# Optimization experiments

Measured on AMD Instinct MI355X. Metric: run time of the kernel, lower is better.

## Reference

```python
import jax, jax.numpy as jnp
import numpy as np

H_G, W_G = 9, 25
N_NODES = H_G * W_G  # 225


def _grid_edge_index():
    # 8-connected grid graph INCLUDING self loops (di=dj=0), matching build_grid_edge_index.
    # PyG GATConv's remove_self_loops+add_self_loops leaves this edge set unchanged.
    edges = []
    for i in range(H_G):
        for j in range(W_G):
            nid = i * W_G + j
            for di in (-1, 0, 1):
                for dj in (-1, 0, 1):
                    ni, nj = i + di, j + dj
                    if 0 <= ni < H_G and 0 <= nj < W_G:
                        edges.append((nid, ni * W_G + nj))
    return jnp.asarray(np.array(edges, dtype=np.int32).T)  # [2, 1825]


def _gat(x, edge_index, W, a_src, a_dst, bias, concat):
    # x: [B, N, F_in]; W: [F_in, heads*d]; a_src/a_dst: [heads, d]
    B = x.shape[0]
    heads, d = a_src.shape
    h = (x @ W).reshape(B, N_NODES, heads, d)          # [B,N,H,D]
    src, dst = edge_index[0], edge_index[1]            # message flows src -> dst
    asrc = jnp.einsum('bnhd,hd->bnh', h, a_src)        # [B,N,H]
    adst = jnp.einsum('bnhd,hd->bnh', h, a_dst)
    e = jax.nn.leaky_relu(asrc[:, src] + adst[:, dst], 0.2)  # [B,E,H]
    et = jnp.transpose(e, (1, 0, 2))                   # [E,B,H] (segment ops over leading axis)
    m = jax.ops.segment_max(et, dst, num_segments=N_NODES)  # [N,B,H]
    ex = jnp.exp(et - m[dst])
    s = jax.ops.segment_sum(ex, dst, num_segments=N_NODES)
    alpha = ex / s[dst]                                # softmax over incoming edges per node
    ht = jnp.transpose(h, (1, 0, 2, 3))                # [N,B,H,D]
    out = jax.ops.segment_sum(alpha[..., None] * ht[src], dst, num_segments=N_NODES)  # [N,B,H,D]
    out = jnp.transpose(out, (1, 0, 2, 3))             # [B,N,H,D]
    if concat:
        out = out.reshape(B, N_NODES, heads * d)
    else:
        out = out.mean(axis=2)
    return out + bias


def setup_inputs() -> dict:
    key = jax.random.key(0)
    ks = jax.random.split(key, 16)
    B = 128
    s = 0.02
    inp = {
        'x4': jax.random.normal(ks[0], (B, 2048, 9, 25), dtype=jnp.float32),
        'pool_w': jax.random.normal(ks[1], (8, 2048), dtype=jnp.float32) * s,
        'pool_b': jnp.zeros((8,), dtype=jnp.float32),
        'gat1_w': jax.random.normal(ks[2], (8, 64), dtype=jnp.float32) * s,
        'gat1_asrc': jax.random.normal(ks[3], (4, 16), dtype=jnp.float32) * s,
        'gat1_adst': jax.random.normal(ks[4], (4, 16), dtype=jnp.float32) * s,
        'gat1_b': jnp.zeros((64,), dtype=jnp.float32),
        'gat2_w': jax.random.normal(ks[5], (64, 8), dtype=jnp.float32) * s,
        'gat2_asrc': jax.random.normal(ks[6], (1, 8), dtype=jnp.float32) * s,
        'gat2_adst': jax.random.normal(ks[7], (1, 8), dtype=jnp.float32) * s,
        'gat2_b': jnp.zeros((8,), dtype=jnp.float32),
        'w1': jax.random.normal(ks[8], (1800, 2048), dtype=jnp.float32) * 0.01,
        'b1': jnp.zeros((2048,), dtype=jnp.float32),
        'w2': jax.random.normal(ks[9], (2048, 20800), dtype=jnp.float32) * 0.01,
        'b2': jnp.zeros((20800,), dtype=jnp.float32),
        'edge_index': _grid_edge_index(),
    }
    return inp


def reference(x4, pool_w, pool_b, gat1_w, gat1_asrc, gat1_adst, gat1_b,
              gat2_w, gat2_asrc, gat2_adst, gat2_b, w1, b1, w2, b2, edge_index):
    B = x4.shape[0]
    # 1x1 conv pool: 2048 -> 8 channels (already 9x25, adaptive_avg_pool2d is identity)
    fea = jnp.einsum('bchw,oc->bohw', x4, pool_w) + pool_b[None, :, None, None]
    fea = fea.reshape(B, 8, N_NODES).transpose(0, 2, 1)  # [B, 225, 8]
    x1 = jax.nn.relu(_gat(fea, edge_index, gat1_w, gat1_asrc, gat1_adst, gat1_b, concat=True))
    x2 = _gat(x1, edge_index, gat2_w, gat2_asrc, gat2_adst, gat2_b, concat=False)  # [B,225,8]
    flat = x2.reshape(B, -1)                             # [B, 1800]
    hid = jax.nn.relu(flat @ w1 + b1)
    out = hid @ w2 + b2
    return out.reshape(-1, 100, 52, 4)
```

## Files before the change

kernel.cpp:

```cpp
#include <hip/hip_runtime.h>
#include <hip/hip_bf16.h>


typedef __attribute__((ext_vector_type(8))) short bh8_t;
typedef __attribute__((ext_vector_type(4))) float f32x4;

static __device__ __forceinline__ short f2bs(float f) {
    __hip_bfloat16 h = __float2bfloat16(f);
    return *reinterpret_cast<short*>(&h);
}
static __device__ __forceinline__ unsigned pack2(short a, short b) {
    return (unsigned)(unsigned short)a | ((unsigned)(unsigned short)b << 16);
}
static __device__ __forceinline__ int swz64(int n, int o) {
    return n * 64 + ((((o >> 2) ^ (n & 15)) << 2) | (o & 3));
}
static __device__ __forceinline__ int swzg(int n, int g) {
    return n * 64 + ((g ^ (n & 15)) << 2);
}

__global__ __launch_bounds__(256) void pool_kernel(const float* __restrict__ x4,
                                                   const float* __restrict__ pool_w,
                                                   float* __restrict__ part) {
    const int b  = blockIdx.x >> 3;
    const int ch = blockIdx.x & 7;
    const int tid = threadIdx.x;
    if (tid >= 225) return;
    const float* xp = x4 + ((size_t)b * 2048 + (size_t)ch * 256) * 225 + tid;
    const float* w0 = pool_w + 0 * 2048 + ch * 256;
    const float* w1 = pool_w + 1 * 2048 + ch * 256;
    const float* w2 = pool_w + 2 * 2048 + ch * 256;
    const float* w3 = pool_w + 3 * 2048 + ch * 256;
    const float* w4 = pool_w + 4 * 2048 + ch * 256;
    const float* w5 = pool_w + 5 * 2048 + ch * 256;
    const float* w6 = pool_w + 6 * 2048 + ch * 256;
    const float* w7 = pool_w + 7 * 2048 + ch * 256;
    float a0 = 0, a1 = 0, a2 = 0, a3 = 0, a4 = 0, a5 = 0, a6 = 0, a7 = 0;
#pragma unroll 8
    for (int c = 0; c < 256; ++c) {
        const float v = xp[c * 225];
        a0 += v * w0[c]; a1 += v * w1[c]; a2 += v * w2[c]; a3 += v * w3[c];
        a4 += v * w4[c]; a5 += v * w5[c]; a6 += v * w6[c]; a7 += v * w7[c];
    }
    float* dst = part + (size_t)b * 14400 + ch * 1800 + tid * 8;
    float4 r0; r0.x = a0; r0.y = a1; r0.z = a2; r0.w = a3;
    float4 r1; r1.x = a4; r1.y = a5; r1.z = a6; r1.w = a7;
    *reinterpret_cast<float4*>(dst) = r0;
    *reinterpret_cast<float4*>(dst + 4) = r1;
}

__global__ __launch_bounds__(256) void gat1_kernel(const float* __restrict__ part,
                                                   const float* __restrict__ pool_b,
                                                   const float* __restrict__ w,
                                                   const float* __restrict__ a_src,
                                                   const float* __restrict__ a_dst,
                                                   const float* __restrict__ bias,
                                                   float* __restrict__ x1) {
    __shared__ __align__(16) float fea[1800];
    __shared__ __align__(16) float h[14400];
    const int b = blockIdx.x;
    const int tid = threadIdx.x;

    for (int i = tid; i < 1800; i += 256) {
        const float* p = part + (size_t)b * 14400 + i;
        float s = 0;
#pragma unroll
        for (int c = 0; c < 8; ++c) s += p[c * 1800];
        fea[i] = s + pool_b[i & 7];
    }
    __syncthreads();

    {
        const int o = tid & 63, mr = tid >> 6;
        float wv[8];
#pragma unroll
        for (int k = 0; k < 8; ++k) wv[k] = w[k * 64 + o];
        for (int n = mr; n < 225; n += 4) {
            float acc = 0;
#pragma unroll
            for (int k = 0; k < 8; ++k) acc += fea[n * 8 + k] * wv[k];
            h[swz64(n, o)] = acc;
        }
    }
    __syncthreads();

    {
        const int hd = tid & 3;
        float4 asw[4], adw[4];
#pragma unroll
        for (int j = 0; j < 4; ++j) {
            asw[j] = *reinterpret_cast<const float4*>(a_src + hd * 16 + 4 * j);
            adw[j] = *reinterpret_cast<const float4*>(a_dst + hd * 16 + 4 * j);
        }
        for (int t = tid; t < 900; t += 256) {
            const int n = t >> 2;
            float as = 0, ad = 0;
#pragma unroll
            for (int j = 0; j < 4; ++j) {
                const float4 hv = *reinterpret_cast<const float4*>(&h[swzg(n, 4 * hd + j)]);
                as += hv.x * asw[j].x + hv.y * asw[j].y + hv.z * asw[j].z + hv.w * asw[j].w;
                ad += hv.x * adw[j].x + hv.y * adw[j].y + hv.z * adw[j].z + hv.w * adw[j].w;
            }
            fea[t] = as;
            fea[900 + t] = ad;
        }
    }
    __syncthreads();

    {
        const int hd = tid & 3;
        float4 b4[4];
#pragma unroll
        for (int j = 0; j < 4; ++j)
            b4[j] = *reinterpret_cast<const float4*>(bias + hd * 16 + 4 * j);
        for (int task = tid; task < 900; task += 256) {
            const int n = task >> 2;
            const int i = n / 25, j25 = n % 25;
            const float adn = fea[900 + task];
            float e[9];
            int sid[9];
            float mx = -1e30f;
#pragma unroll
            for (int t9 = 0; t9 < 9; ++t9) {
                const int di = t9 / 3 - 1, dj = t9 % 3 - 1;
                const int ni = i + di, nj = j25 + dj;
                const bool valid = ((unsigned)ni < 9u) && ((unsigned)nj < 25u);
                const int s = valid ? ni * 25 + nj : n;
                sid[t9] = s;
                float ev = fea[s * 4 + hd] + adn;
                ev = ev >= 0.f ? ev : 0.2f * ev;
                e[t9] = valid ? ev : -1e30f;
                mx = fmaxf(mx, e[t9]);
            }
            float sum = 0;
#pragma unroll
            for (int t9 = 0; t9 < 9; ++t9) {
                float ex = __expf(e[t9] - mx);
                e[t9] = ex;
                sum += ex;
            }
            const float inv = 1.f / sum;
            float4 o4[4] = {};
#pragma unroll
            for (int t9 = 0; t9 < 9; ++t9) {
                const float al = e[t9] * inv;
                const int s = sid[t9];
#pragma unroll
                for (int jj = 0; jj < 4; ++jj) {
                    const float4 hv = *reinterpret_cast<const float4*>(&h[swzg(s, 4 * hd + jj)]);
                    o4[jj].x += al * hv.x; o4[jj].y += al * hv.y;
                    o4[jj].z += al * hv.z; o4[jj].w += al * hv.w;
                }
            }
            float* dst = x1 + (size_t)b * 14400 + n * 64 + hd * 16;
#pragma unroll
            for (int jj = 0; jj < 4; ++jj) {
                float4 r;
                r.x = fmaxf(o4[jj].x + b4[jj].x, 0.f);
                r.y = fmaxf(o4[jj].y + b4[jj].y, 0.f);
                r.z = fmaxf(o4[jj].z + b4[jj].z, 0.f);
                r.w = fmaxf(o4[jj].w + b4[jj].w, 0.f);
                *reinterpret_cast<float4*>(dst + 4 * jj) = r;
            }
        }
    }
}

__global__ __launch_bounds__(256) void gat2_kernel(const float* __restrict__ x1,
                                                   const float* __restrict__ w,
                                                   const float* __restrict__ a_src,
                                                   const float* __restrict__ a_dst,
                                                   const float* __restrict__ bias,
                                                   short* __restrict__ flat) {
    __shared__ __align__(16) float xs[14400];
    __shared__ __align__(16) float h2[8 * 232];
    const int b = blockIdx.x;
    const int tid = threadIdx.x;
    for (int i4 = tid; i4 < 3600; i4 += 256) {
        const int n = i4 >> 4, g0 = i4 & 15;
        const float4 v = *reinterpret_cast<const float4*>(&x1[(size_t)b * 14400 + (i4 << 2)]);
        *reinterpret_cast<float4*>(&xs[swzg(n, g0)]) = v;
    }
    __syncthreads();
    for (int t = tid; t < 1800; t += 256) {
        const int o = t & 7, n = t >> 3;
        float acc = 0;
#pragma unroll
        for (int jj = 0; jj < 16; ++jj) {
            const float4 xv = *reinterpret_cast<const float4*>(&xs[swzg(n, jj)]);
            const int k = 4 * jj;
            acc += xv.x * w[k * 8 + o] + xv.y * w[(k + 1) * 8 + o]
                 + xv.z * w[(k + 2) * 8 + o] + xv.w * w[(k + 3) * 8 + o];
        }
        h2[o * 232 + n] = acc;
    }
    __syncthreads();
    if (tid < 225) {
        const int n = tid, i = n / 25, j = n % 25;
        float av[8], dv[8];
#pragma unroll
        for (int d = 0; d < 8; ++d) { av[d] = a_src[d]; dv[d] = a_dst[d]; }
        float adn = 0;
#pragma unroll
        for (int d = 0; d < 8; ++d) adn += h2[d * 232 + n] * dv[d];
        float e[9];
        int sid[9];
        float mx = -1e30f;
#pragma unroll
        for (int t9 = 0; t9 < 9; ++t9) {
            const int di = t9 / 3 - 1, dj = t9 % 3 - 1;
            const int ni = i + di, nj = j + dj;
            const bool valid = ((unsigned)ni < 9u) && ((unsigned)nj < 25u);
            const int s = valid ? ni * 25 + nj : n;
            sid[t9] = s;
            float as = 0;
#pragma unroll
            for (int d = 0; d < 8; ++d) as += h2[d * 232 + s] * av[d];
            float ev = as + adn;
            ev = ev >= 0.f ? ev : 0.2f * ev;
            e[t9] = valid ? ev : -1e30f;
            mx = fmaxf(mx, e[t9]);
        }
        float sum = 0;
#pragma unroll
        for (int t9 = 0; t9 < 9; ++t9) {
            float ex = __expf(e[t9] - mx);
            e[t9] = ex;
            sum += ex;
        }
        const float inv = 1.f / sum;
        float out[8] = {};
#pragma unroll
        for (int t9 = 0; t9 < 9; ++t9) {
            const float al = e[t9] * inv;
#pragma unroll
            for (int d = 0; d < 8; ++d) out[d] += al * h2[d * 232 + sid[t9]];
        }
        unsigned u[4];
#pragma unroll
        for (int p = 0; p < 4; ++p)
            u[p] = pack2(f2bs(out[2 * p] + bias[2 * p]), f2bs(out[2 * p + 1] + bias[2 * p + 1]));
        uint4 uv; uv.x = u[0]; uv.y = u[1]; uv.z = u[2]; uv.w = u[3];
        *reinterpret_cast<uint4*>(flat + (size_t)b * 1800 + n * 8) = uv;
    }
}

template <int BN, int MT, int NT, int NWN, bool RELU, bool OUT_BF16>
__global__ __launch_bounds__(256) void gemm_mfma(const short* __restrict__ A,
                                                 const float* __restrict__ Wf,
                                                 const float* __restrict__ bias,
                                                 void* __restrict__ outp,
                                                 int K, int N) {
    constexpr int LDT = 40;
    constexpr int EPT = (32 * BN) / 256;
    __shared__ __align__(16) short sA[128 * LDT];
    __shared__ __align__(16) short sB[BN * LDT];
    const int tid = threadIdx.x;
    const int lane = tid & 63;
    const int wave = tid >> 6;
    const int n0 = blockIdx.x * BN;
    const int wm0 = (wave / NWN) * (MT * 16);
    const int wn0 = (wave % NWN) * (NT * 16);
    const int lm = lane & 15;
    const int lkb = (lane >> 4) * 8;

    const int am = tid >> 1;
    const int akh = tid & 1;
    const int bn_ = tid % BN;
    const int bk0 = (tid / BN) * EPT;

    union { uint4 v[2]; short s[16]; } pa;
    float pb[EPT];
    const int nkt = (K + 31) >> 5;

    auto loadg = [&](int kt) {
        const int k0 = kt << 5;
        if (k0 + 32 <= K) {
            const uint4* src = reinterpret_cast<const uint4*>(A + (size_t)am * K + k0 + akh * 16);
            pa.v[0] = src[0];
            pa.v[1] = src[1];
#pragma unroll
            for (int jj = 0; jj < EPT; ++jj)
                pb[jj] = Wf[(size_t)(k0 + bk0 + jj) * N + n0 + bn_];
        } else {
#pragma unroll
            for (int jj = 0; jj < 16; ++jj) {
                const int kk = k0 + akh * 16 + jj;
                pa.s[jj] = (kk < K) ? A[(size_t)am * K + kk] : (short)0;
            }
#pragma unroll
            for (int jj = 0; jj < EPT; ++jj) {
                const int kk = k0 + bk0 + jj;
                pb[jj] = (kk < K) ? Wf[(size_t)kk * N + n0 + bn_] : 0.f;
            }
        }
    };

    f32x4 acc[MT][NT] = {};
    loadg(0);

    for (int kt = 0; kt < nkt; ++kt) {
        __syncthreads();
        {
            uint4* dstA = reinterpret_cast<uint4*>(&sA[am * LDT + akh * 16]);
            dstA[0] = pa.v[0];
            dstA[1] = pa.v[1];
            unsigned uw[EPT / 2];
#pragma unroll
            for (int jj = 0; jj < EPT / 2; ++jj)
                uw[jj] = pack2(f2bs(pb[2 * jj]), f2bs(pb[2 * jj + 1]));
            short* bdst = &sB[bn_ * LDT + bk0];
            if constexpr (EPT == 8) {
                uint4 u; u.x = uw[0]; u.y = uw[1]; u.z = uw[2]; u.w = uw[3];
                *reinterpret_cast<uint4*>(bdst) = u;
            } else if constexpr (EPT == 4) {
                uint2 u; u.x = uw[0]; u.y = uw[1];
                *reinterpret_cast<uint2*>(bdst) = u;
            } else {
                *reinterpret_cast<unsigned*>(bdst) = uw[0];
            }
        }
        __syncthreads();
        if (kt + 1 < nkt) loadg(kt + 1);
        bh8_t bfr[NT];
#pragma unroll
        for (int nt = 0; nt < NT; ++nt)
            bfr[nt] = *reinterpret_cast<const bh8_t*>(&sB[(wn0 + nt * 16 + lm) * LDT + lkb]);
#pragma unroll
        for (int mt = 0; mt < MT; ++mt) {
            bh8_t afr = *reinterpret_cast<const bh8_t*>(&sA[(wm0 + mt * 16 + lm) * LDT + lkb]);
#pragma unroll
            for (int nt = 0; nt < NT; ++nt)
                acc[mt][nt] = __builtin_amdgcn_mfma_f32_16x16x32_bf16(afr, bfr[nt], acc[mt][nt], 0, 0, 0);
        }
    }
    const int rg = lane >> 4;
#pragma unroll
    for (int nt = 0; nt < NT; ++nt) {
        const int n = n0 + wn0 + nt * 16 + lm;
        const float bv = bias[n];
#pragma unroll
        for (int mt = 0; mt < MT; ++mt) {
#pragma unroll
            for (int r = 0; r < 4; ++r) {
                const int m = wm0 + mt * 16 + rg * 4 + r;
                float v = acc[mt][nt][r] + bv;
                if (RELU) v = fmaxf(v, 0.f);
                if (OUT_BF16)
                    reinterpret_cast<short*>(outp)[(size_t)m * N + n] = f2bs(v);
                else
                    reinterpret_cast<float*>(outp)[(size_t)m * N + n] = v;
            }
        }
    }
}

extern "C" void kernel_launch(void* const* d_in, const int* in_sizes, int n_in,
                              void* d_out, int out_size, void* d_ws, size_t ws_size,
                              hipStream_t stream) {
    const float* x4        = (const float*)d_in[0];
    const float* pool_w    = (const float*)d_in[1];
    const float* pool_b    = (const float*)d_in[2];
    const float* gat1_w    = (const float*)d_in[3];
    const float* gat1_asrc = (const float*)d_in[4];
    const float* gat1_adst = (const float*)d_in[5];
    const float* gat1_b    = (const float*)d_in[6];
    const float* gat2_w    = (const float*)d_in[7];
    const float* gat2_asrc = (const float*)d_in[8];
    const float* gat2_adst = (const float*)d_in[9];
    const float* gat2_b    = (const float*)d_in[10];
    const float* w1        = (const float*)d_in[11];
    const float* b1        = (const float*)d_in[12];
    const float* w2        = (const float*)d_in[13];
    const float* b2        = (const float*)d_in[14];
    float* out = (float*)d_out;

    char* ws = (char*)d_ws;
    float* part = (float*)ws;
    float* x1   = (float*)(ws + 7372800);
    short* flat = (short*)(ws + 14745600);
    short* hid  = (short*)(ws + 15206400);

    pool_kernel<<<1024, 256, 0, stream>>>(x4, pool_w, part);
    gat1_kernel<<<128, 256, 0, stream>>>(part, pool_b, gat1_w, gat1_asrc, gat1_adst, gat1_b, x1);
    gat2_kernel<<<128, 256, 0, stream>>>(x1, gat2_w, gat2_asrc, gat2_adst, gat2_b, flat);
    gemm_mfma<16, 2, 1, 1, true, true><<<128, 256, 0, stream>>>(flat, w1, b1, (void*)hid, 1800, 2048);
    gemm_mfma<32, 4, 1, 2, false, false><<<650, 256, 0, stream>>>(hid, w2, b2, (void*)out, 2048, 20800);
}
```

Measured before the change: 577.7 us.

## Split-K the first FC GEMM with a reduce kernel and retile the second

The first dense layer (K=1800, N=2048) now runs split-K across 4 slices, growing the grid from 128 to 512 blocks. Each slice writes fp32 partials, and a new reduce kernel sums them, adds the bias, applies ReLU and converts to bf16. The second GEMM moves from a 32-wide to a 16-wide N tile with one wave column, doubling its grid to 1300 blocks. This trades fewer idle CUs for extra partial-sum traffic, one more launch, and smaller tiles that reuse the A operand less.

```diff
diff --git a/kernel.cpp b/kernel.cpp
--- a/kernel.cpp
+++ b/kernel.cpp
@@ -245,12 +245,12 @@
     }
 }
 
-template <int BN, int MT, int NT, int NWN, bool RELU, bool OUT_BF16>
+template <int BN, int MT, int NT, int NWN, int NSPLIT, bool RELU, bool OUT_BF16, bool HAS_BIAS>
 __global__ __launch_bounds__(256) void gemm_mfma(const short* __restrict__ A,
                                                  const float* __restrict__ Wf,
                                                  const float* __restrict__ bias,
                                                  void* __restrict__ outp,
-                                                 int K, int N) {
+                                                 int K, int N, int kps) {
     constexpr int LDT = 40;
     constexpr int EPT = (32 * BN) / 256;
     __shared__ __align__(16) short sA[128 * LDT];
@@ -258,7 +258,9 @@
     const int tid = threadIdx.x;
     const int lane = tid & 63;
     const int wave = tid >> 6;
-    const int n0 = blockIdx.x * BN;
+    const int spl  = blockIdx.x & (NSPLIT - 1);
+    const int nblk = blockIdx.x / NSPLIT;
+    const int n0 = nblk * BN;
     const int wm0 = (wave / NWN) * (MT * 16);
     const int wn0 = (wave % NWN) * (NT * 16);
     const int lm = lane & 15;
@@ -272,6 +274,8 @@
     union { uint4 v[2]; short s[16]; } pa;
     float pb[EPT];
     const int nkt = (K + 31) >> 5;
+    const int kt0 = spl * kps;
+    const int kt1 = (kt0 + kps < nkt) ? kt0 + kps : nkt;
 
     auto loadg = [&](int kt) {
         const int k0 = kt << 5;
@@ -297,9 +301,9 @@
     };
 
     f32x4 acc[MT][NT] = {};
-    loadg(0);
-
-    for (int kt = 0; kt < nkt; ++kt) {
+    loadg(kt0);
+
+    for (int kt = kt0; kt < kt1; ++kt) {
         __syncthreads();
         {
             uint4* dstA = reinterpret_cast<uint4*>(&sA[am * LDT + akh * 16]);
@@ -321,7 +325,7 @@
             }
         }
         __syncthreads();
-        if (kt + 1 < nkt) loadg(kt + 1);
+        if (kt + 1 < kt1) loadg(kt + 1);
         bh8_t bfr[NT];
 #pragma unroll
         for (int nt = 0; nt < NT; ++nt)
@@ -338,7 +342,7 @@
 #pragma unroll
     for (int nt = 0; nt < NT; ++nt) {
         const int n = n0 + wn0 + nt * 16 + lm;
-        const float bv = bias[n];
+        const float bv = HAS_BIAS ? bias[n] : 0.f;
 #pragma unroll
         for (int mt = 0; mt < MT; ++mt) {
 #pragma unroll
@@ -349,10 +353,31 @@
                 if (OUT_BF16)
                     reinterpret_cast<short*>(outp)[(size_t)m * N + n] = f2bs(v);
                 else
-                    reinterpret_cast<float*>(outp)[(size_t)m * N + n] = v;
-            }
-        }
-    }
+                    reinterpret_cast<float*>(outp)[((size_t)spl * 128 + m) * N + n] = v;
+            }
+        }
+    }
+}
+
+__global__ __launch_bounds__(256) void fc1_reduce_kernel(const float* __restrict__ part4,
+                                                         const float* __restrict__ b1,
+                                                         short* __restrict__ hid) {
+    const int g = blockIdx.x * 256 + threadIdx.x;
+    const float4* p = reinterpret_cast<const float4*>(part4);
+    float4 a = p[g];
+    const float4 v1 = p[g + 65536];
+    const float4 v2 = p[g + 131072];
+    const float4 v3 = p[g + 196608];
+    const int e = g << 2;
+    const float4 bv = *reinterpret_cast<const float4*>(b1 + (e & 2047));
+    a.x = fmaxf(a.x + v1.x + v2.x + v3.x + bv.x, 0.f);
+    a.y = fmaxf(a.y + v1.y + v2.y + v3.y + bv.y, 0.f);
+    a.z = fmaxf(a.z + v1.z + v2.z + v3.z + bv.z, 0.f);
+    a.w = fmaxf(a.w + v1.w + v2.w + v3.w + bv.w, 0.f);
+    uint2 u;
+    u.x = pack2(f2bs(a.x), f2bs(a.y));
+    u.y = pack2(f2bs(a.z), f2bs(a.w));
+    *reinterpret_cast<uint2*>(hid + e) = u;
 }
 
 extern "C" void kernel_launch(void* const* d_in, const int* in_sizes, int n_in,
@@ -376,14 +401,18 @@
     float* out = (float*)d_out;
 
     char* ws = (char*)d_ws;
-    float* part = (float*)ws;
-    float* x1   = (float*)(ws + 7372800);
-    short* flat = (short*)(ws + 14745600);
-    short* hid  = (short*)(ws + 15206400);
+    float* part  = (float*)ws;
+    float* x1    = (float*)(ws + 7372800);
+    short* flat  = (short*)(ws + 14745600);
+    short* hid   = (short*)(ws + 15206400);
+    float* fc1p  = (float*)(ws + 15730688);
 
     pool_kernel<<<1024, 256, 0, stream>>>(x4, pool_w, part);
     gat1_kernel<<<128, 256, 0, stream>>>(part, pool_b, gat1_w, gat1_asrc, gat1_adst, gat1_b, x1);
     gat2_kernel<<<128, 256, 0, stream>>>(x1, gat2_w, gat2_asrc, gat2_adst, gat2_b, flat);
-    gemm_mfma<16, 2, 1, 1, true, true><<<128, 256, 0, stream>>>(flat, w1, b1, (void*)hid, 1800, 2048);
-    gemm_mfma<32, 4, 1, 2, false, false><<<650, 256, 0, stream>>>(hid, w2, b2, (void*)out, 2048, 20800);
-}
+    gemm_mfma<16, 2, 1, 1, 4, false, false, false>
+        <<<512, 256, 0, stream>>>(flat, w1, nullptr, (void*)fc1p, 1800, 2048, 15);
+    fc1_reduce_kernel<<<256, 256, 0, stream>>>(fc1p, b1, hid);
+    gemm_mfma<16, 2, 1, 1, 1, false, false, true>
+        <<<1300, 256, 0, stream>>>(hid, w2, b2, (void*)out, 2048, 20800, 64);
+}
```

Measured after the change: 580.5 us. Within noise of the previous version (+0.5%).
